# Kernel optimization log

Measured on AMD Instinct MI355X. Metric: run time of the kernel, lower is better.

The kernel has to match this reference:

```python
import jax, jax.numpy as jnp
import numpy as np

N_NODES = 100000
N_EDGES = 1600000
D_FEAT = 64
NUM_LAYERS = 4  # -> num_gcn_layers = 3


def spmm(edge_row, edge_col, edge_vals, x, n_nodes):
    # out[r] = sum_{e: row[e]==r} vals[e] * x[col[e]]
    gathered = edge_vals[:, None] * x[edge_col]  # [E, d]
    return jax.ops.segment_sum(gathered, edge_row, num_segments=n_nodes)


def setup_inputs() -> dict:
    key = jax.random.key(0)
    k1, k2, k3, k4 = jax.random.split(key, 4)
    x = jax.random.normal(k1, (N_NODES, D_FEAT), dtype=jnp.float32)
    edge_row = jax.random.randint(k2, (N_EDGES,), 0, N_NODES, dtype=jnp.int32)
    edge_col = jax.random.randint(k3, (N_EDGES,), 0, N_NODES, dtype=jnp.int32)
    edge_vals = jax.random.uniform(k4, (N_EDGES,), dtype=jnp.float32)
    return {"x": x, "edge_row": edge_row, "edge_col": edge_col, "edge_vals": edge_vals}


def reference(x, edge_row, edge_col, edge_vals):
    # resSumGCN: h_{i+1} = A h_i ; return sum_{i=1..L} h_i
    num_gcn_layers = NUM_LAYERS - 1
    h = x
    acc = jnp.zeros_like(x)
    for _ in range(num_gcn_layers):  # small fixed layer count
        h = spmm(edge_row, edge_col, edge_vals, h, N_NODES)
        acc = acc + h
    return acc
```

## Files before the change

### kernel.cpp

```cpp
#include <hip/hip_runtime.h>

#define N_NODES 100000
#define N_EDGES 1600000
#define D_FEAT  64

#define RSHIFT 8
#define RPB    256
#define NBK    ((N_NODES + RPB - 1) / RPB)
#define CAP    5120
#define EPB    4096
#define KBLK   ((N_EDGES + EPB - 1) / EPB)
#define OROW   (NBK + 1)
#define CVB    ((N_NODES * D_FEAT / 4 + 1023) / 1024)

typedef float f32x2 __attribute__((ext_vector_type(2)));

__device__ __forceinline__ unsigned short f2bf(float f) {
  union { float f; unsigned int i; } v; v.f = f;
  unsigned int b = v.i;
  return (unsigned short)((b + 0x7FFFu + ((b >> 16) & 1u)) >> 16);
}
__device__ __forceinline__ float ulo(int u) { return __int_as_float(u << 16); }
__device__ __forceinline__ float uhi(int u) { return __int_as_float(u & 0xFFFF0000); }
__device__ __forceinline__ f32x2 upk(int u) {
  f32x2 r; r.x = ulo(u); r.y = uhi(u); return r;
}
__device__ __forceinline__ int pk(float a, float b) {
  return (int)f2bf(a) | ((int)f2bf(b) << 16);
}

__global__ __launch_bounds__(1024) void convert_bin(
    const float4* __restrict__ xin, ushort4* __restrict__ xout,
    const int* __restrict__ erow, const int* __restrict__ ecol,
    const float* __restrict__ evals, int2* __restrict__ tmp,
    int* __restrict__ offs) {
  __shared__ int hist[NBK];
  __shared__ int sc[NBK];
  int t = threadIdx.x;
  int k = blockIdx.x;
  if (k >= KBLK) {
    int i = (k - KBLK) * 1024 + t;
    if (i < N_NODES * D_FEAT / 4) {
      float4 v = xin[i];
      ushort4 o;
      o.x = f2bf(v.x); o.y = f2bf(v.y); o.z = f2bf(v.z); o.w = f2bf(v.w);
      xout[i] = o;
    }
    return;
  }
  if (t < NBK) hist[t] = 0;
  __syncthreads();
  int base = k * EPB;
  int nk = N_EDGES - base; if (nk > EPB) nk = EPB;
  int key[4], vb[4], rk[4], bk[4];
#pragma unroll
  for (int j = 0; j < 4; ++j) {
    int li = j * 1024 + t;
    bk[j] = -1;
    if (li < nk) {
      int e = base + li;
      int r = erow[e];
      key[j] = ((r & (RPB - 1)) << 17) | ecol[e];
      vb[j]  = __float_as_int(evals[e]);
      bk[j]  = r >> RSHIFT;
      rk[j]  = atomicAdd(&hist[bk[j]], 1);
    }
  }
  __syncthreads();
  if (t < NBK) sc[t] = hist[t];
  __syncthreads();
  for (int off = 1; off < NBK; off <<= 1) {
    int u = (t >= off && t < NBK) ? sc[t - off] : 0;
    __syncthreads();
    if (t < NBK) sc[t] += u;
    __syncthreads();
  }
  if (t < NBK) {
    int ex = sc[t] - hist[t];
    sc[t] = ex;
    offs[k * OROW + t] = ex;
  }
  if (t == 0) offs[k * OROW + NBK] = nk;
  __syncthreads();
#pragma unroll
  for (int j = 0; j < 4; ++j) {
    if (bk[j] >= 0) {
      int pos = sc[bk[j]] + rk[j];
      tmp[k * EPB + pos] = make_int2(key[j], vb[j]);
    }
  }
}

__global__ __launch_bounds__(256) void build_csr(
    const int2* __restrict__ tmp, const int* __restrict__ offs,
    int2* __restrict__ edges, int* __restrict__ row_beg,
    int* __restrict__ row_end) {
  __shared__ int hist[RPB];
  __shared__ int cur[RPB];
  int b = blockIdx.x;
  int t = threadIdx.x;
  int oct = t >> 3;
  int ol  = t & 7;
  hist[t] = 0;
  __syncthreads();
  for (int k = oct; k < KBLK; k += 32) {
    int o0 = offs[k * OROW + b];
    int o1 = offs[k * OROW + b + 1];
    const int2* seg = tmp + k * EPB;
    for (int i = o0 + ol; i < o1; i += 8)
      atomicAdd(&hist[seg[i].x >> 17], 1);
  }
  __syncthreads();
  int v  = hist[t];
  int v2 = (v + 1) & ~1;
  cur[t] = v2;
  __syncthreads();
  for (int off = 1; off < 256; off <<= 1) {
    int u = (t >= off) ? cur[t - off] : 0;
    __syncthreads();
    cur[t] += u;
    __syncthreads();
  }
  int excl2 = cur[t] - v2;
  int base = b * CAP;
  int gr = b * RPB + t;
  if (gr < N_NODES) {
    row_beg[gr] = base + excl2;
    row_end[gr] = base + excl2 + v;
  }
  if (v & 1) edges[base + excl2 + v] = make_int2(0, 0);
  __syncthreads();
  cur[t] = excl2;
  __syncthreads();
  for (int k = oct; k < KBLK; k += 32) {
    int o0 = offs[k * OROW + b];
    int o1 = offs[k * OROW + b + 1];
    const int2* seg = tmp + k * EPB;
    for (int i = o0 + ol; i < o1; i += 8) {
      int2 ed = seg[i];
      int pos = atomicAdd(&cur[ed.x >> 17], 1);
      edges[base + pos] = make_int2(ed.x & 0x1FFFF, ed.y);
    }
  }
}

__global__ __launch_bounds__(256) void spmm_wave(
    const int* __restrict__ row_beg, const int* __restrict__ row_end,
    const int2* __restrict__ edges, const int4* __restrict__ xq,
    int4* __restrict__ h_q, float4* __restrict__ out,
    const int4* __restrict__ add1, const int4* __restrict__ add2,
    int final_mode) {
  int t = threadIdx.x;
  int lane = t & 63;
  int oct = lane >> 3;
  int ol  = lane & 7;
  int row = blockIdx.x * 4 + (t >> 6);
  int e0 = row_beg[row];
  int e1 = row_end[row];
  const int4* ebase = (const int4*)edges;
  f32x2 c0 = {0.f, 0.f}, c1 = {0.f, 0.f}, c2 = {0.f, 0.f}, c3 = {0.f, 0.f};

#define WIN(p) { \
    int4 m = ebase[(p) + oct]; \
    int4 g0 = xq[(size_t)m.x * 8 + ol]; \
    int4 g1 = xq[(size_t)m.z * 8 + ol]; \
    float v0 = __int_as_float(m.y), v1 = __int_as_float(m.w); \
    f32x2 vv0 = {v0, v0}, vv1 = {v1, v1}; \
    c0 += vv0 * upk(g0.x) + vv1 * upk(g1.x); \
    c1 += vv0 * upk(g0.y) + vv1 * upk(g1.y); \
    c2 += vv0 * upk(g0.z) + vv1 * upk(g1.z); \
    c3 += vv0 * upk(g0.w) + vv1 * upk(g1.w); \
  }

  int nw = (e1 - e0) >> 4;
  int e = e0;
  int it = 0;
  for (; it + 2 <= nw; it += 2, e += 32) {
    int p = e >> 1;
    WIN(p);
    WIN(p + 8);
  }
  if (it < nw) { WIN(e >> 1); e += 16; }
  int pairs = (e1 - e + 1) >> 1;
  if (oct < pairs) { WIN(e >> 1); }
#undef WIN

#pragma unroll
  for (int m = 8; m < 64; m <<= 1) {
    c0.x += __shfl_xor(c0.x, m, 64); c0.y += __shfl_xor(c0.y, m, 64);
    c1.x += __shfl_xor(c1.x, m, 64); c1.y += __shfl_xor(c1.y, m, 64);
    c2.x += __shfl_xor(c2.x, m, 64); c2.y += __shfl_xor(c2.y, m, 64);
    c3.x += __shfl_xor(c3.x, m, 64); c3.y += __shfl_xor(c3.y, m, 64);
  }
  if (oct == 0) {
    size_t oi = (size_t)row * 8 + ol;
    if (final_mode) {
      int4 r1 = add1[oi];
      int4 r2 = add2[oi];
      float4 lo, hi;
      lo.x = c0.x + ulo(r1.x) + ulo(r2.x);
      lo.y = c0.y + uhi(r1.x) + uhi(r2.x);
      lo.z = c1.x + ulo(r1.y) + ulo(r2.y);
      lo.w = c1.y + uhi(r1.y) + uhi(r2.y);
      hi.x = c2.x + ulo(r1.z) + ulo(r2.z);
      hi.y = c2.y + uhi(r1.z) + uhi(r2.z);
      hi.z = c3.x + ulo(r1.w) + ulo(r2.w);
      hi.w = c3.y + uhi(r1.w) + uhi(r2.w);
      out[(size_t)row * 16 + ol * 2]     = lo;
      out[(size_t)row * 16 + ol * 2 + 1] = hi;
    } else {
      int4 p;
      p.x = pk(c0.x, c0.y);
      p.y = pk(c1.x, c1.y);
      p.z = pk(c2.x, c2.y);
      p.w = pk(c3.x, c3.y);
      h_q[oi] = p;
    }
  }
}

extern "C" void kernel_launch(void* const* d_in, const int* in_sizes, int n_in,
                              void* d_out, int out_size, void* d_ws, size_t ws_size,
                              hipStream_t stream) {
  const float* x     = (const float*)d_in[0];
  const int*   erow  = (const int*)d_in[1];
  const int*   ecol  = (const int*)d_in[2];
  const float* evals = (const float*)d_in[3];
  float* out = (float*)d_out;

  const size_t hb_bytes   = (size_t)N_NODES * D_FEAT * 2;
  const size_t ecap_bytes = (size_t)NBK * CAP * sizeof(int2);
  char* ws = (char*)d_ws;
  int4*    xbf  = (int4*)   (ws);
  int4*    bufA = (int4*)   (ws + hb_bytes);
  int2*    tmp  = (int2*)   (ws + hb_bytes);
  int4*    bufB = (int4*)   (ws + 2 * hb_bytes);
  int*     offs = (int*)    (ws + 2 * hb_bytes);
  int2* edges   = (int2*)(ws + 3 * hb_bytes);
  int* row_beg  = (int*) (ws + 3 * hb_bytes + ecap_bytes);
  int* row_end  = (int*) (ws + 3 * hb_bytes + ecap_bytes + 400000);

  const int sblocks = N_NODES / 4;

  convert_bin<<<KBLK + CVB, 1024, 0, stream>>>(
      (const float4*)x, (ushort4*)xbf, erow, ecol, evals, tmp, offs);
  build_csr<<<NBK, 256, 0, stream>>>(tmp, offs, edges, row_beg, row_end);

  spmm_wave<<<sblocks, 256, 0, stream>>>(row_beg, row_end, edges, xbf,
                                         bufA, nullptr, nullptr, nullptr, 0);
  spmm_wave<<<sblocks, 256, 0, stream>>>(row_beg, row_end, edges, bufA,
                                         bufB, nullptr, nullptr, nullptr, 0);
  spmm_wave<<<sblocks, 256, 0, stream>>>(row_beg, row_end, edges, bufB,
                                         nullptr, (float4*)out, bufA, bufB, 1);
}
```

Before: 244.7 us.

## Assign one row per 8-lane group instead of one row per wavefront in SpMM

The SpMM kernel now maps each 8-lane octet to its own row, so a 64-lane wave handles 8 rows and a block handles 32. Each octet walks its row's edge pairs serially, which removes the cross-octet shuffle reduction and the idle lanes on short rows (average degree about 16). In exchange each octet runs a longer serial loop, with fewer independent gathers in flight per row, and load imbalance between rows of different degree now shows up within a wave. The grid shrinks from N/4 to N/32 blocks; N_NODES is divisible by 32, so the row indexing stays in bounds.

Result: faster. 225.7 us (-7.8%).

```diff
diff --git a/kernel.cpp b/kernel.cpp
--- a/kernel.cpp
+++ b/kernel.cpp
@@ -144,7 +144,7 @@
   }
 }
 
-__global__ __launch_bounds__(256) void spmm_wave(
+__global__ __launch_bounds__(256) void spmm_oct(
     const int* __restrict__ row_beg, const int* __restrict__ row_end,
     const int2* __restrict__ edges, const int4* __restrict__ xq,
     int4* __restrict__ h_q, float4* __restrict__ out,
@@ -154,17 +154,17 @@
   int lane = t & 63;
   int oct = lane >> 3;
   int ol  = lane & 7;
-  int row = blockIdx.x * 4 + (t >> 6);
+  int row = blockIdx.x * 32 + (t >> 6) * 8 + oct;
   int e0 = row_beg[row];
   int e1 = row_end[row];
-  const int4* ebase = (const int4*)edges;
+  const int4* ep = (const int4*)edges + (e0 >> 1);
+  int npair = (e1 - e0 + 1) >> 1;
   f32x2 c0 = {0.f, 0.f}, c1 = {0.f, 0.f}, c2 = {0.f, 0.f}, c3 = {0.f, 0.f};
 
-#define WIN(p) { \
-    int4 m = ebase[(p) + oct]; \
-    int4 g0 = xq[(size_t)m.x * 8 + ol]; \
-    int4 g1 = xq[(size_t)m.z * 8 + ol]; \
-    float v0 = __int_as_float(m.y), v1 = __int_as_float(m.w); \
+#define PAIR(m) { \
+    int4 g0 = xq[(size_t)(m).x * 8 + ol]; \
+    int4 g1 = xq[(size_t)(m).z * 8 + ol]; \
+    float v0 = __int_as_float((m).y), v1 = __int_as_float((m).w); \
     f32x2 vv0 = {v0, v0}, vv1 = {v1, v1}; \
     c0 += vv0 * upk(g0.x) + vv1 * upk(g1.x); \
     c1 += vv0 * upk(g0.y) + vv1 * upk(g1.y); \
@@ -172,50 +172,41 @@
     c3 += vv0 * upk(g0.w) + vv1 * upk(g1.w); \
   }
 
-  int nw = (e1 - e0) >> 4;
-  int e = e0;
-  int it = 0;
-  for (; it + 2 <= nw; it += 2, e += 32) {
-    int p = e >> 1;
-    WIN(p);
-    WIN(p + 8);
-  }
-  if (it < nw) { WIN(e >> 1); e += 16; }
-  int pairs = (e1 - e + 1) >> 1;
-  if (oct < pairs) { WIN(e >> 1); }
-#undef WIN
-
-#pragma unroll
-  for (int m = 8; m < 64; m <<= 1) {
-    c0.x += __shfl_xor(c0.x, m, 64); c0.y += __shfl_xor(c0.y, m, 64);
-    c1.x += __shfl_xor(c1.x, m, 64); c1.y += __shfl_xor(c1.y, m, 64);
-    c2.x += __shfl_xor(c2.x, m, 64); c2.y += __shfl_xor(c2.y, m, 64);
-    c3.x += __shfl_xor(c3.x, m, 64); c3.y += __shfl_xor(c3.y, m, 64);
-  }
-  if (oct == 0) {
-    size_t oi = (size_t)row * 8 + ol;
-    if (final_mode) {
-      int4 r1 = add1[oi];
-      int4 r2 = add2[oi];
-      float4 lo, hi;
-      lo.x = c0.x + ulo(r1.x) + ulo(r2.x);
-      lo.y = c0.y + uhi(r1.x) + uhi(r2.x);
-      lo.z = c1.x + ulo(r1.y) + ulo(r2.y);
-      lo.w = c1.y + uhi(r1.y) + uhi(r2.y);
-      hi.x = c2.x + ulo(r1.z) + ulo(r2.z);
-      hi.y = c2.y + uhi(r1.z) + uhi(r2.z);
-      hi.z = c3.x + ulo(r1.w) + ulo(r2.w);
-      hi.w = c3.y + uhi(r1.w) + uhi(r2.w);
-      out[(size_t)row * 16 + ol * 2]     = lo;
-      out[(size_t)row * 16 + ol * 2 + 1] = hi;
-    } else {
-      int4 p;
-      p.x = pk(c0.x, c0.y);
-      p.y = pk(c1.x, c1.y);
-      p.z = pk(c2.x, c2.y);
-      p.w = pk(c3.x, c3.y);
-      h_q[oi] = p;
-    }
+  int p = 0;
+  for (; p + 2 <= npair; p += 2) {
+    int4 m0 = ep[p];
+    int4 m1 = ep[p + 1];
+    PAIR(m0);
+    PAIR(m1);
+  }
+  if (p < npair) {
+    int4 m0 = ep[p];
+    PAIR(m0);
+  }
+#undef PAIR
+
+  size_t oi = (size_t)row * 8 + ol;
+  if (final_mode) {
+    int4 r1 = add1[oi];
+    int4 r2 = add2[oi];
+    float4 lo, hi;
+    lo.x = c0.x + ulo(r1.x) + ulo(r2.x);
+    lo.y = c0.y + uhi(r1.x) + uhi(r2.x);
+    lo.z = c1.x + ulo(r1.y) + ulo(r2.y);
+    lo.w = c1.y + uhi(r1.y) + uhi(r2.y);
+    hi.x = c2.x + ulo(r1.z) + ulo(r2.z);
+    hi.y = c2.y + uhi(r1.z) + uhi(r2.z);
+    hi.z = c3.x + ulo(r1.w) + ulo(r2.w);
+    hi.w = c3.y + uhi(r1.w) + uhi(r2.w);
+    out[(size_t)row * 16 + ol * 2]     = lo;
+    out[(size_t)row * 16 + ol * 2 + 1] = hi;
+  } else {
+    int4 pq;
+    pq.x = pk(c0.x, c0.y);
+    pq.y = pk(c1.x, c1.y);
+    pq.z = pk(c2.x, c2.y);
+    pq.w = pk(c3.x, c3.y);
+    h_q[oi] = pq;
   }
 }
 
@@ -240,16 +231,16 @@
   int* row_beg  = (int*) (ws + 3 * hb_bytes + ecap_bytes);
   int* row_end  = (int*) (ws + 3 * hb_bytes + ecap_bytes + 400000);
 
-  const int sblocks = N_NODES / 4;
+  const int sblocks = N_NODES / 32;
 
   convert_bin<<<KBLK + CVB, 1024, 0, stream>>>(
       (const float4*)x, (ushort4*)xbf, erow, ecol, evals, tmp, offs);
   build_csr<<<NBK, 256, 0, stream>>>(tmp, offs, edges, row_beg, row_end);
 
-  spmm_wave<<<sblocks, 256, 0, stream>>>(row_beg, row_end, edges, xbf,
-                                         bufA, nullptr, nullptr, nullptr, 0);
-  spmm_wave<<<sblocks, 256, 0, stream>>>(row_beg, row_end, edges, bufA,
-                                         bufB, nullptr, nullptr, nullptr, 0);
-  spmm_wave<<<sblocks, 256, 0, stream>>>(row_beg, row_end, edges, bufB,
-                                         nullptr, (float4*)out, bufA, bufB, 1);
-}
+  spmm_oct<<<sblocks, 256, 0, stream>>>(row_beg, row_end, edges, xbf,
+                                        bufA, nullptr, nullptr, nullptr, 0);
+  spmm_oct<<<sblocks, 256, 0, stream>>>(row_beg, row_end, edges, bufA,
+                                        bufB, nullptr, nullptr, nullptr, 0);
+  spmm_oct<<<sblocks, 256, 0, stream>>>(row_beg, row_end, edges, bufB,
+                                        nullptr, (float4*)out, bufA, bufB, 1);
+}
```
